# Kernel optimization log

Measured on AMD Instinct MI355X. Metric: run time of the kernel, lower is better.

Reference implementation:

```python
import jax, jax.numpy as jnp
import numpy as np

T, K, N = 4096, 4096, 11008
EPS = 1e-5


def setup_inputs() -> dict:
    key = jax.random.key(0)
    k1, k2, k3, k4 = jax.random.split(key, 4)
    input_tensor = jax.random.normal(k1, (1, T, K), dtype=jnp.bfloat16)
    # int8 weights in [-127, 127]
    weight = jax.random.randint(k2, (N, K), -127, 128, dtype=jnp.int8)
    # per-output-channel weight scale, small positive values
    weight_scale = (jax.random.uniform(k3, (N, 1), dtype=jnp.float32) * 0.02 + 1e-4)
    bias = jax.random.normal(k4, (N,), dtype=jnp.bfloat16)
    return {"input_tensor": input_tensor, "weight": weight,
            "weight_scale": weight_scale, "bias": bias}


def _quantize_per_token_absmax(x):
    # x: [T, K] float -> int8 quant [T, K], float32 scale [T, 1]
    xf = x.astype(jnp.float32)
    absmax = jnp.max(jnp.abs(xf), axis=-1, keepdims=True)  # [T, 1]
    scale = jnp.maximum(absmax, EPS) / 127.0
    q = jnp.clip(jnp.round(xf / scale), -127, 127).astype(jnp.int8)
    return q, scale


def reference(input_tensor, weight, weight_scale, bias):
    x = jnp.squeeze(input_tensor, axis=0)                  # [T, K]
    x_q, x_scale = _quantize_per_token_absmax(x)           # int8 [T,K], f32 [T,1]
    # int8 GEMM with int32 accumulation: [T, K] @ [K, N]
    acc = jax.lax.dot_general(
        x_q, weight.T,
        dimension_numbers=(((1,), (0,)), ((), ())),
        preferred_element_type=jnp.int32,
    )
    # dequantize: per-token scale * per-channel scale
    out = (acc.astype(jnp.float32) * x_scale * weight_scale.T).astype(jnp.bfloat16)
    out = out + bias
    return out[None, :, :]                                  # [1, T, N]
```

## Files before the change

kernel.cpp:

```cpp
#include <hip/hip_runtime.h>
#include <hip/hip_bf16.h>
#include <stdint.h>

#define T_DIM 4096
#define K_DIM 4096
#define N_DIM 11008

#define XQ_OFF 0
#define XS_OFF 16777216
#define W8_OFF 16793600

typedef __attribute__((ext_vector_type(4))) int v4i;

__global__ __launch_bounds__(256) void quant_kernel(
    const float* __restrict__ x, int8_t* __restrict__ xq, float* __restrict__ xs)
{
    const int wid   = threadIdx.x >> 6;
    const int lane  = threadIdx.x & 63;
    const int token = blockIdx.x * 4 + wid;

    const float* xrow = x + (size_t)token * K_DIM;

    float4 v[16];
    float am = 0.0f;
#pragma unroll
    for (int j = 0; j < 16; ++j) {
        v[j] = *(const float4*)(xrow + (size_t)(j * 64 + lane) * 4);
        am = fmaxf(am, fmaxf(fmaxf(fabsf(v[j].x), fabsf(v[j].y)),
                             fmaxf(fabsf(v[j].z), fabsf(v[j].w))));
    }
#pragma unroll
    for (int m = 1; m < 64; m <<= 1)
        am = fmaxf(am, __shfl_xor(am, m, 64));

    const float scale = fmaxf(am, 1e-5f) / 127.0f;
    if (lane == 0) xs[token] = scale;

    uint32_t* qrow = (uint32_t*)(xq + (size_t)token * K_DIM);
#pragma unroll
    for (int j = 0; j < 16; ++j) {
        int q0 = min(127, max(-127, (int)rintf(v[j].x / scale)));
        int q1 = min(127, max(-127, (int)rintf(v[j].y / scale)));
        int q2 = min(127, max(-127, (int)rintf(v[j].z / scale)));
        int q3 = min(127, max(-127, (int)rintf(v[j].w / scale)));
        qrow[j * 64 + lane] = ((uint32_t)(uint8_t)(int8_t)q0)       |
                              ((uint32_t)(uint8_t)(int8_t)q1 << 8)  |
                              ((uint32_t)(uint8_t)(int8_t)q2 << 16) |
                              ((uint32_t)(uint8_t)(int8_t)q3 << 24);
    }
}

__global__ __launch_bounds__(256) void pack_w_kernel(
    const int* __restrict__ w32, int8_t* __restrict__ w8)
{
    const size_t tid = (size_t)blockIdx.x * 256 + threadIdx.x;
    const int4* src = (const int4*)w32 + tid * 4;
    uint32_t o[4];
#pragma unroll
    for (int i = 0; i < 4; ++i) {
        int4 a = src[i];
        o[i] = ((uint32_t)a.x & 0xFFu) | (((uint32_t)a.y & 0xFFu) << 8) |
               (((uint32_t)a.z & 0xFFu) << 16) | ((uint32_t)a.w << 24);
    }
    *(uint4*)(w8 + tid * 16) = make_uint4(o[0], o[1], o[2], o[3]);
}

#define BM 256
#define BN 256
#define BKB 64
#define NT (K_DIM / BKB)
#define BUF_SZ 16384

__global__ __launch_bounds__(512, 2) void gemm_i8_kernel(
    const int8_t* __restrict__ xq, const int8_t* __restrict__ w8,
    const float* __restrict__ xs, const float* __restrict__ wsc,
    const __hip_bfloat16* __restrict__ bias, float* __restrict__ out)
{
    __shared__ int8_t lds[3 * 2 * BUF_SZ];

    constexpr int NBN = N_DIM / BN;
    constexpr int NWG = (T_DIM / BM) * NBN;
    constexpr int CPX = NWG / 8;

    const int bid = blockIdx.x;
    const int b2  = (bid % 8) * CPX + bid / 8;
    const int bm  = b2 / NBN;
    const int bn  = b2 % NBN;

    const int tid  = threadIdx.x;
    const int wid  = tid >> 6;
    const int lane = tid & 63;
    const int wm   = wid >> 2;
    const int wn   = wid & 3;

    const int fr = lane & 15, kg = lane >> 4;
    int offA[8], offB[4];
#pragma unroll
    for (int mi = 0; mi < 8; ++mi) {
        const int row = wm * 128 + mi * 16 + fr;
        offA[mi] = row * 64 + ((kg ^ ((row >> 1) & 3)) << 4);
    }
#pragma unroll
    for (int ni = 0; ni < 4; ++ni) {
        const int row = wn * 64 + ni * 16 + fr;
        offB[ni] = row * 64 + ((kg ^ ((row >> 1) & 3)) << 4);
    }

    const int srow  = tid >> 2;
    const int sslot = tid & 3;
    const int r0 = srow, r1 = 128 + srow;
    const int c0 = sslot ^ ((r0 >> 1) & 3);
    const int c1 = sslot ^ ((r1 >> 1) & 3);
    const int8_t* gA0 = xq + (size_t)(bm * BM + r0) * K_DIM + c0 * 16;
    const int8_t* gA1 = xq + (size_t)(bm * BM + r1) * K_DIM + c1 * 16;
    const int8_t* gB0 = w8 + (size_t)(bn * BM + r0) * K_DIM + c0 * 16;
    const int8_t* gB1 = w8 + (size_t)(bn * BM + r1) * K_DIM + c1 * 16;
    const int ldsW = wid * 1024;

    v4i acc[8][4];
#pragma unroll
    for (int mi = 0; mi < 8; ++mi)
#pragma unroll
        for (int ni = 0; ni < 4; ++ni) acc[mi][ni] = (v4i){0, 0, 0, 0};

#define STAGE(bufb, mat, Rr, kt)                                                \
    __builtin_amdgcn_global_load_lds(                                           \
        (const __attribute__((address_space(1))) void*)(                        \
            ((mat) ? ((Rr) ? gB1 : gB0) : ((Rr) ? gA1 : gA0)) +                 \
            (size_t)(kt) * BKB),                                                \
        (__attribute__((address_space(3))) void*)(                              \
            lds + ((bufb) * 2 + (mat)) * BUF_SZ + (Rr) * 8192 + ldsW),          \
        16, 0, 0)

    STAGE(0, 0, 0, 0); STAGE(0, 0, 1, 0); STAGE(0, 1, 0, 0); STAGE(0, 1, 1, 0);
    STAGE(1, 0, 0, 1); STAGE(1, 0, 1, 1); STAGE(1, 1, 0, 1); STAGE(1, 1, 1, 1);
    asm volatile("s_waitcnt vmcnt(4)" ::: "memory");
    __builtin_amdgcn_s_barrier();
    asm volatile("" ::: "memory");

    for (int t = 0; t < NT; ++t) {
        const int b  = t % 3;
        const int pb = (t + 2) % 3;
        const int8_t* bA = lds + (b * 2 + 0) * BUF_SZ;
        const int8_t* bB = lds + (b * 2 + 1) * BUF_SZ;

        v4i bF[4], aF[4];
#pragma unroll
        for (int ni = 0; ni < 4; ++ni) bF[ni] = *(const v4i*)(bB + offB[ni]);
#pragma unroll
        for (int mi = 0; mi < 4; ++mi) aF[mi] = *(const v4i*)(bA + offA[mi]);
        if (t + 2 < NT) { STAGE(pb, 0, 0, t + 2); STAGE(pb, 0, 1, t + 2); }
        __builtin_amdgcn_s_barrier();
        asm volatile("" ::: "memory");
        __builtin_amdgcn_s_setprio(1);
#pragma unroll
        for (int mi = 0; mi < 4; ++mi)
#pragma unroll
            for (int ni = 0; ni < 4; ++ni)
                acc[mi][ni] = __builtin_amdgcn_mfma_i32_16x16x64_i8(
                    aF[mi], bF[ni], acc[mi][ni], 0, 0, 0);
        __builtin_amdgcn_s_setprio(0);
        __builtin_amdgcn_s_barrier();
        asm volatile("" ::: "memory");

#pragma unroll
        for (int mi = 0; mi < 4; ++mi) aF[mi] = *(const v4i*)(bA + offA[mi + 4]);
        if (t + 2 < NT) { STAGE(pb, 1, 0, t + 2); STAGE(pb, 1, 1, t + 2); }
        __builtin_amdgcn_s_barrier();
        asm volatile("" ::: "memory");
        __builtin_amdgcn_s_setprio(1);
#pragma unroll
        for (int mi = 0; mi < 4; ++mi)
#pragma unroll
            for (int ni = 0; ni < 4; ++ni)
                acc[mi + 4][ni] = __builtin_amdgcn_mfma_i32_16x16x64_i8(
                    aF[mi], bF[ni], acc[mi + 4][ni], 0, 0, 0);
        __builtin_amdgcn_s_setprio(0);
        if (t < NT - 2) asm volatile("s_waitcnt vmcnt(4)" ::: "memory");
        else            asm volatile("s_waitcnt vmcnt(0)" ::: "memory");
        __builtin_amdgcn_s_barrier();
        asm volatile("" ::: "memory");
    }

    const int row0 = bm * BM + wm * 128 + (lane >> 4) * 4;
    const int col0 = bn * BN + wn * 64 + (lane & 15);
#pragma unroll
    for (int mi = 0; mi < 8; ++mi) {
#pragma unroll
        for (int j = 0; j < 4; ++j) {
            const int row = row0 + mi * 16 + j;
            const float xscale = xs[row];
#pragma unroll
            for (int ni = 0; ni < 4; ++ni) {
                const int col = col0 + ni * 16;
                float p   = (float)acc[mi][ni][j] * xscale * wsc[col];
                float pb_ = __bfloat162float(__float2bfloat16(p));
                float vb  = __bfloat162float(__float2bfloat16(
                                pb_ + __bfloat162float(bias[col])));
                out[(size_t)row * N_DIM + col] = vb;
            }
        }
    }
#undef STAGE
}

extern "C" void kernel_launch(void* const* d_in, const int* in_sizes, int n_in,
                              void* d_out, int out_size, void* d_ws, size_t ws_size,
                              hipStream_t stream)
{
    const float*          x    = (const float*)d_in[0];
    const int*            w32  = (const int*)d_in[1];
    const float*          wsc  = (const float*)d_in[2];
    const __hip_bfloat16* bias = (const __hip_bfloat16*)d_in[3];
    float*                out  = (float*)d_out;

    int8_t* xq = (int8_t*)d_ws + XQ_OFF;
    float*  xs = (float*)((char*)d_ws + XS_OFF);
    int8_t* w8 = (int8_t*)d_ws + W8_OFF;

    quant_kernel<<<T_DIM / 4, 256, 0, stream>>>(x, xq, xs);
    pack_w_kernel<<<(N_DIM * (K_DIM / 16)) / 256, 256, 0, stream>>>(w32, w8);
    gemm_i8_kernel<<<(T_DIM / BM) * (N_DIM / BN), 512, 0, stream>>>(
        xq, w8, xs, wsc, bias, out);
}
```

Measured before the change: 275.0 us.

## Merge prep kernels and split GEMM k-step into four finer MFMA phases

Combines the activation quantization and weight packing kernels into one launch, with blocks dispatched by index, so one launch overhead and the gap between the two kernels go away. The GEMM main loop moves from two phases of 16 MFMAs to four phases of 8 MFMAs. Each phase issues one global-to-LDS prefetch and loads two A fragments, which spreads the memory traffic more evenly across the compute and lowers A-fragment register use. The cost is twice as many workgroup barriers per k-step, which may hurt MFMA throughput.

New measurement: 269.4 us. -2.0%, faster.

```diff
diff --git a/kernel.cpp b/kernel.cpp
--- a/kernel.cpp
+++ b/kernel.cpp
@@ -12,57 +12,56 @@
 
 typedef __attribute__((ext_vector_type(4))) int v4i;
 
-__global__ __launch_bounds__(256) void quant_kernel(
-    const float* __restrict__ x, int8_t* __restrict__ xq, float* __restrict__ xs)
-{
-    const int wid   = threadIdx.x >> 6;
-    const int lane  = threadIdx.x & 63;
-    const int token = blockIdx.x * 4 + wid;
-
-    const float* xrow = x + (size_t)token * K_DIM;
-
-    float4 v[16];
-    float am = 0.0f;
-#pragma unroll
-    for (int j = 0; j < 16; ++j) {
-        v[j] = *(const float4*)(xrow + (size_t)(j * 64 + lane) * 4);
-        am = fmaxf(am, fmaxf(fmaxf(fabsf(v[j].x), fabsf(v[j].y)),
-                             fmaxf(fabsf(v[j].z), fabsf(v[j].w))));
-    }
-#pragma unroll
-    for (int m = 1; m < 64; m <<= 1)
-        am = fmaxf(am, __shfl_xor(am, m, 64));
-
-    const float scale = fmaxf(am, 1e-5f) / 127.0f;
-    if (lane == 0) xs[token] = scale;
-
-    uint32_t* qrow = (uint32_t*)(xq + (size_t)token * K_DIM);
-#pragma unroll
-    for (int j = 0; j < 16; ++j) {
-        int q0 = min(127, max(-127, (int)rintf(v[j].x / scale)));
-        int q1 = min(127, max(-127, (int)rintf(v[j].y / scale)));
-        int q2 = min(127, max(-127, (int)rintf(v[j].z / scale)));
-        int q3 = min(127, max(-127, (int)rintf(v[j].w / scale)));
-        qrow[j * 64 + lane] = ((uint32_t)(uint8_t)(int8_t)q0)       |
-                              ((uint32_t)(uint8_t)(int8_t)q1 << 8)  |
-                              ((uint32_t)(uint8_t)(int8_t)q2 << 16) |
-                              ((uint32_t)(uint8_t)(int8_t)q3 << 24);
-    }
-}
-
-__global__ __launch_bounds__(256) void pack_w_kernel(
+__global__ __launch_bounds__(256) void prep_kernel(
+    const float* __restrict__ x, int8_t* __restrict__ xq, float* __restrict__ xs,
     const int* __restrict__ w32, int8_t* __restrict__ w8)
 {
-    const size_t tid = (size_t)blockIdx.x * 256 + threadIdx.x;
-    const int4* src = (const int4*)w32 + tid * 4;
-    uint32_t o[4];
-#pragma unroll
-    for (int i = 0; i < 4; ++i) {
-        int4 a = src[i];
-        o[i] = ((uint32_t)a.x & 0xFFu) | (((uint32_t)a.y & 0xFFu) << 8) |
-               (((uint32_t)a.z & 0xFFu) << 16) | ((uint32_t)a.w << 24);
-    }
-    *(uint4*)(w8 + tid * 16) = make_uint4(o[0], o[1], o[2], o[3]);
+    if (blockIdx.x < T_DIM / 4) {
+        const int wid   = threadIdx.x >> 6;
+        const int lane  = threadIdx.x & 63;
+        const int token = blockIdx.x * 4 + wid;
+
+        const float* xrow = x + (size_t)token * K_DIM;
+
+        float4 v[16];
+        float am = 0.0f;
+#pragma unroll
+        for (int j = 0; j < 16; ++j) {
+            v[j] = *(const float4*)(xrow + (size_t)(j * 64 + lane) * 4);
+            am = fmaxf(am, fmaxf(fmaxf(fabsf(v[j].x), fabsf(v[j].y)),
+                                 fmaxf(fabsf(v[j].z), fabsf(v[j].w))));
+        }
+#pragma unroll
+        for (int m = 1; m < 64; m <<= 1)
+            am = fmaxf(am, __shfl_xor(am, m, 64));
+
+        const float scale = fmaxf(am, 1e-5f) / 127.0f;
+        if (lane == 0) xs[token] = scale;
+
+        uint32_t* qrow = (uint32_t*)(xq + (size_t)token * K_DIM);
+#pragma unroll
+        for (int j = 0; j < 16; ++j) {
+            int q0 = min(127, max(-127, (int)rintf(v[j].x / scale)));
+            int q1 = min(127, max(-127, (int)rintf(v[j].y / scale)));
+            int q2 = min(127, max(-127, (int)rintf(v[j].z / scale)));
+            int q3 = min(127, max(-127, (int)rintf(v[j].w / scale)));
+            qrow[j * 64 + lane] = ((uint32_t)(uint8_t)(int8_t)q0)       |
+                                  ((uint32_t)(uint8_t)(int8_t)q1 << 8)  |
+                                  ((uint32_t)(uint8_t)(int8_t)q2 << 16) |
+                                  ((uint32_t)(uint8_t)(int8_t)q3 << 24);
+        }
+    } else {
+        const size_t tid = (size_t)(blockIdx.x - T_DIM / 4) * 256 + threadIdx.x;
+        const int4* src = (const int4*)w32 + tid * 4;
+        uint32_t o[4];
+#pragma unroll
+        for (int i = 0; i < 4; ++i) {
+            int4 a = src[i];
+            o[i] = ((uint32_t)a.x & 0xFFu) | (((uint32_t)a.y & 0xFFu) << 8) |
+                   (((uint32_t)a.z & 0xFFu) << 16) | ((uint32_t)a.w << 24);
+        }
+        *(uint4*)(w8 + tid * 16) = make_uint4(o[0], o[1], o[2], o[3]);
+    }
 }
 
 #define BM 256
@@ -132,6 +131,14 @@
             lds + ((bufb) * 2 + (mat)) * BUF_SZ + (Rr) * 8192 + ldsW),          \
         16, 0, 0)
 
+#define MFMA_PAIR(base)                                                         \
+    _Pragma("unroll")                                                           \
+    for (int mi = 0; mi < 2; ++mi)                                              \
+        _Pragma("unroll")                                                       \
+        for (int ni = 0; ni < 4; ++ni)                                          \
+            acc[(base) + mi][ni] = __builtin_amdgcn_mfma_i32_16x16x64_i8(       \
+                aF[mi], bF[ni], acc[(base) + mi][ni], 0, 0, 0)
+
     STAGE(0, 0, 0, 0); STAGE(0, 0, 1, 0); STAGE(0, 1, 0, 0); STAGE(0, 1, 1, 0);
     STAGE(1, 0, 0, 1); STAGE(1, 0, 1, 1); STAGE(1, 1, 0, 1); STAGE(1, 1, 1, 1);
     asm volatile("s_waitcnt vmcnt(4)" ::: "memory");
@@ -143,38 +150,52 @@
         const int pb = (t + 2) % 3;
         const int8_t* bA = lds + (b * 2 + 0) * BUF_SZ;
         const int8_t* bB = lds + (b * 2 + 1) * BUF_SZ;
-
-        v4i bF[4], aF[4];
+        const bool pf = (t + 2 < NT);
+
+        v4i bF[4], aF[2];
+
 #pragma unroll
         for (int ni = 0; ni < 4; ++ni) bF[ni] = *(const v4i*)(bB + offB[ni]);
-#pragma unroll
-        for (int mi = 0; mi < 4; ++mi) aF[mi] = *(const v4i*)(bA + offA[mi]);
-        if (t + 2 < NT) { STAGE(pb, 0, 0, t + 2); STAGE(pb, 0, 1, t + 2); }
-        __builtin_amdgcn_s_barrier();
-        asm volatile("" ::: "memory");
-        __builtin_amdgcn_s_setprio(1);
-#pragma unroll
-        for (int mi = 0; mi < 4; ++mi)
-#pragma unroll
-            for (int ni = 0; ni < 4; ++ni)
-                acc[mi][ni] = __builtin_amdgcn_mfma_i32_16x16x64_i8(
-                    aF[mi], bF[ni], acc[mi][ni], 0, 0, 0);
-        __builtin_amdgcn_s_setprio(0);
-        __builtin_amdgcn_s_barrier();
-        asm volatile("" ::: "memory");
-
-#pragma unroll
-        for (int mi = 0; mi < 4; ++mi) aF[mi] = *(const v4i*)(bA + offA[mi + 4]);
-        if (t + 2 < NT) { STAGE(pb, 1, 0, t + 2); STAGE(pb, 1, 1, t + 2); }
-        __builtin_amdgcn_s_barrier();
-        asm volatile("" ::: "memory");
-        __builtin_amdgcn_s_setprio(1);
-#pragma unroll
-        for (int mi = 0; mi < 4; ++mi)
-#pragma unroll
-            for (int ni = 0; ni < 4; ++ni)
-                acc[mi + 4][ni] = __builtin_amdgcn_mfma_i32_16x16x64_i8(
-                    aF[mi], bF[ni], acc[mi + 4][ni], 0, 0, 0);
+        aF[0] = *(const v4i*)(bA + offA[0]);
+        aF[1] = *(const v4i*)(bA + offA[1]);
+        if (pf) STAGE(pb, 0, 0, t + 2);
+        __builtin_amdgcn_s_barrier();
+        asm volatile("" ::: "memory");
+        __builtin_amdgcn_s_setprio(1);
+        MFMA_PAIR(0);
+        __builtin_amdgcn_s_setprio(0);
+        __builtin_amdgcn_s_barrier();
+        asm volatile("" ::: "memory");
+
+        aF[0] = *(const v4i*)(bA + offA[2]);
+        aF[1] = *(const v4i*)(bA + offA[3]);
+        if (pf) STAGE(pb, 0, 1, t + 2);
+        __builtin_amdgcn_s_barrier();
+        asm volatile("" ::: "memory");
+        __builtin_amdgcn_s_setprio(1);
+        MFMA_PAIR(2);
+        __builtin_amdgcn_s_setprio(0);
+        __builtin_amdgcn_s_barrier();
+        asm volatile("" ::: "memory");
+
+        aF[0] = *(const v4i*)(bA + offA[4]);
+        aF[1] = *(const v4i*)(bA + offA[5]);
+        if (pf) STAGE(pb, 1, 0, t + 2);
+        __builtin_amdgcn_s_barrier();
+        asm volatile("" ::: "memory");
+        __builtin_amdgcn_s_setprio(1);
+        MFMA_PAIR(4);
+        __builtin_amdgcn_s_setprio(0);
+        __builtin_amdgcn_s_barrier();
+        asm volatile("" ::: "memory");
+
+        aF[0] = *(const v4i*)(bA + offA[6]);
+        aF[1] = *(const v4i*)(bA + offA[7]);
+        if (pf) STAGE(pb, 1, 1, t + 2);
+        __builtin_amdgcn_s_barrier();
+        asm volatile("" ::: "memory");
+        __builtin_amdgcn_s_setprio(1);
+        MFMA_PAIR(6);
         __builtin_amdgcn_s_setprio(0);
         if (t < NT - 2) asm volatile("s_waitcnt vmcnt(4)" ::: "memory");
         else            asm volatile("s_waitcnt vmcnt(0)" ::: "memory");
@@ -193,8 +214,8 @@
 #pragma unroll
             for (int ni = 0; ni < 4; ++ni) {
                 const int col = col0 + ni * 16;
-                float p   = (float)acc[mi][ni][j] * xscale * wsc[col];
-                float pb_ = __bfloat162float(__float2bfloat16(p));
+                float p_  = (float)acc[mi][ni][j] * xscale * wsc[col];
+                float pb_ = __bfloat162float(__float2bfloat16(p_));
                 float vb  = __bfloat162float(__float2bfloat16(
                                 pb_ + __bfloat162float(bias[col])));
                 out[(size_t)row * N_DIM + col] = vb;
@@ -202,6 +223,7 @@
         }
     }
 #undef STAGE
+#undef MFMA_PAIR
 }
 
 extern "C" void kernel_launch(void* const* d_in, const int* in_sizes, int n_in,
@@ -218,8 +240,8 @@
     float*  xs = (float*)((char*)d_ws + XS_OFF);
     int8_t* w8 = (int8_t*)d_ws + W8_OFF;
 
-    quant_kernel<<<T_DIM / 4, 256, 0, stream>>>(x, xq, xs);
-    pack_w_kernel<<<(N_DIM * (K_DIM / 16)) / 256, 256, 0, stream>>>(w32, w8);
+    prep_kernel<<<T_DIM / 4 + (N_DIM * (K_DIM / 16)) / 256, 256, 0, stream>>>(
+        x, xq, xs, w32, w8);
     gemm_i8_kernel<<<(T_DIM / BM) * (N_DIM / BN), 512, 0, stream>>>(
         xq, w8, xs, wsc, bias, out);
 }
```

## Merge prep kernels and collapse GEMM main loop into single-phase schedule

Applied to the files above, without the earlier changes.

Activation quantization and weight packing move into one prep kernel whose blocks branch on block index, which removes one launch and lets both jobs run concurrently. The GEMM inner loop drops its two-phase split with four barriers per K-tile. It now issues all four global-to-LDS prefetches up front, loads all A and B fragments, runs the 32 MFMAs, and then waits once before a single barrier. This cuts barrier overhead but holds eight A fragments live at once, which raises register pressure and gives less interleaving of LDS reads with MFMA work.

Result: faster. 264.7 us (-3.8%).

```diff
diff --git a/kernel.cpp b/kernel.cpp
--- a/kernel.cpp
+++ b/kernel.cpp
@@ -12,57 +12,56 @@
 
 typedef __attribute__((ext_vector_type(4))) int v4i;
 
-__global__ __launch_bounds__(256) void quant_kernel(
-    const float* __restrict__ x, int8_t* __restrict__ xq, float* __restrict__ xs)
-{
-    const int wid   = threadIdx.x >> 6;
-    const int lane  = threadIdx.x & 63;
-    const int token = blockIdx.x * 4 + wid;
-
-    const float* xrow = x + (size_t)token * K_DIM;
-
-    float4 v[16];
-    float am = 0.0f;
-#pragma unroll
-    for (int j = 0; j < 16; ++j) {
-        v[j] = *(const float4*)(xrow + (size_t)(j * 64 + lane) * 4);
-        am = fmaxf(am, fmaxf(fmaxf(fabsf(v[j].x), fabsf(v[j].y)),
-                             fmaxf(fabsf(v[j].z), fabsf(v[j].w))));
-    }
-#pragma unroll
-    for (int m = 1; m < 64; m <<= 1)
-        am = fmaxf(am, __shfl_xor(am, m, 64));
-
-    const float scale = fmaxf(am, 1e-5f) / 127.0f;
-    if (lane == 0) xs[token] = scale;
-
-    uint32_t* qrow = (uint32_t*)(xq + (size_t)token * K_DIM);
-#pragma unroll
-    for (int j = 0; j < 16; ++j) {
-        int q0 = min(127, max(-127, (int)rintf(v[j].x / scale)));
-        int q1 = min(127, max(-127, (int)rintf(v[j].y / scale)));
-        int q2 = min(127, max(-127, (int)rintf(v[j].z / scale)));
-        int q3 = min(127, max(-127, (int)rintf(v[j].w / scale)));
-        qrow[j * 64 + lane] = ((uint32_t)(uint8_t)(int8_t)q0)       |
-                              ((uint32_t)(uint8_t)(int8_t)q1 << 8)  |
-                              ((uint32_t)(uint8_t)(int8_t)q2 << 16) |
-                              ((uint32_t)(uint8_t)(int8_t)q3 << 24);
-    }
-}
-
-__global__ __launch_bounds__(256) void pack_w_kernel(
+__global__ __launch_bounds__(256) void prep_kernel(
+    const float* __restrict__ x, int8_t* __restrict__ xq, float* __restrict__ xs,
     const int* __restrict__ w32, int8_t* __restrict__ w8)
 {
-    const size_t tid = (size_t)blockIdx.x * 256 + threadIdx.x;
-    const int4* src = (const int4*)w32 + tid * 4;
-    uint32_t o[4];
-#pragma unroll
-    for (int i = 0; i < 4; ++i) {
-        int4 a = src[i];
-        o[i] = ((uint32_t)a.x & 0xFFu) | (((uint32_t)a.y & 0xFFu) << 8) |
-               (((uint32_t)a.z & 0xFFu) << 16) | ((uint32_t)a.w << 24);
-    }
-    *(uint4*)(w8 + tid * 16) = make_uint4(o[0], o[1], o[2], o[3]);
+    if (blockIdx.x < T_DIM / 4) {
+        const int wid   = threadIdx.x >> 6;
+        const int lane  = threadIdx.x & 63;
+        const int token = blockIdx.x * 4 + wid;
+
+        const float* xrow = x + (size_t)token * K_DIM;
+
+        float4 v[16];
+        float am = 0.0f;
+#pragma unroll
+        for (int j = 0; j < 16; ++j) {
+            v[j] = *(const float4*)(xrow + (size_t)(j * 64 + lane) * 4);
+            am = fmaxf(am, fmaxf(fmaxf(fabsf(v[j].x), fabsf(v[j].y)),
+                                 fmaxf(fabsf(v[j].z), fabsf(v[j].w))));
+        }
+#pragma unroll
+        for (int m = 1; m < 64; m <<= 1)
+            am = fmaxf(am, __shfl_xor(am, m, 64));
+
+        const float scale = fmaxf(am, 1e-5f) / 127.0f;
+        if (lane == 0) xs[token] = scale;
+
+        uint32_t* qrow = (uint32_t*)(xq + (size_t)token * K_DIM);
+#pragma unroll
+        for (int j = 0; j < 16; ++j) {
+            int q0 = min(127, max(-127, (int)rintf(v[j].x / scale)));
+            int q1 = min(127, max(-127, (int)rintf(v[j].y / scale)));
+            int q2 = min(127, max(-127, (int)rintf(v[j].z / scale)));
+            int q3 = min(127, max(-127, (int)rintf(v[j].w / scale)));
+            qrow[j * 64 + lane] = ((uint32_t)(uint8_t)(int8_t)q0)       |
+                                  ((uint32_t)(uint8_t)(int8_t)q1 << 8)  |
+                                  ((uint32_t)(uint8_t)(int8_t)q2 << 16) |
+                                  ((uint32_t)(uint8_t)(int8_t)q3 << 24);
+        }
+    } else {
+        const size_t tid = (size_t)(blockIdx.x - T_DIM / 4) * 256 + threadIdx.x;
+        const int4* src = (const int4*)w32 + tid * 4;
+        uint32_t o[4];
+#pragma unroll
+        for (int i = 0; i < 4; ++i) {
+            int4 a = src[i];
+            o[i] = ((uint32_t)a.x & 0xFFu) | (((uint32_t)a.y & 0xFFu) << 8) |
+                   (((uint32_t)a.z & 0xFFu) << 16) | ((uint32_t)a.w << 24);
+        }
+        *(uint4*)(w8 + tid * 16) = make_uint4(o[0], o[1], o[2], o[3]);
+    }
 }
 
 #define BM 256
@@ -144,38 +143,26 @@
         const int8_t* bA = lds + (b * 2 + 0) * BUF_SZ;
         const int8_t* bB = lds + (b * 2 + 1) * BUF_SZ;
 
-        v4i bF[4], aF[4];
+        if (t + 2 < NT) {
+            STAGE(pb, 0, 0, t + 2); STAGE(pb, 0, 1, t + 2);
+            STAGE(pb, 1, 0, t + 2); STAGE(pb, 1, 1, t + 2);
+        }
+
+        v4i bF[4], aF[8];
 #pragma unroll
         for (int ni = 0; ni < 4; ++ni) bF[ni] = *(const v4i*)(bB + offB[ni]);
 #pragma unroll
-        for (int mi = 0; mi < 4; ++mi) aF[mi] = *(const v4i*)(bA + offA[mi]);
-        if (t + 2 < NT) { STAGE(pb, 0, 0, t + 2); STAGE(pb, 0, 1, t + 2); }
-        __builtin_amdgcn_s_barrier();
-        asm volatile("" ::: "memory");
+        for (int mi = 0; mi < 8; ++mi) aF[mi] = *(const v4i*)(bA + offA[mi]);
+
         __builtin_amdgcn_s_setprio(1);
 #pragma unroll
-        for (int mi = 0; mi < 4; ++mi)
+        for (int mi = 0; mi < 8; ++mi)
 #pragma unroll
             for (int ni = 0; ni < 4; ++ni)
                 acc[mi][ni] = __builtin_amdgcn_mfma_i32_16x16x64_i8(
                     aF[mi], bF[ni], acc[mi][ni], 0, 0, 0);
         __builtin_amdgcn_s_setprio(0);
-        __builtin_amdgcn_s_barrier();
-        asm volatile("" ::: "memory");
-
-#pragma unroll
-        for (int mi = 0; mi < 4; ++mi) aF[mi] = *(const v4i*)(bA + offA[mi + 4]);
-        if (t + 2 < NT) { STAGE(pb, 1, 0, t + 2); STAGE(pb, 1, 1, t + 2); }
-        __builtin_amdgcn_s_barrier();
-        asm volatile("" ::: "memory");
-        __builtin_amdgcn_s_setprio(1);
-#pragma unroll
-        for (int mi = 0; mi < 4; ++mi)
-#pragma unroll
-            for (int ni = 0; ni < 4; ++ni)
-                acc[mi + 4][ni] = __builtin_amdgcn_mfma_i32_16x16x64_i8(
-                    aF[mi], bF[ni], acc[mi + 4][ni], 0, 0, 0);
-        __builtin_amdgcn_s_setprio(0);
+
         if (t < NT - 2) asm volatile("s_waitcnt vmcnt(4)" ::: "memory");
         else            asm volatile("s_waitcnt vmcnt(0)" ::: "memory");
         __builtin_amdgcn_s_barrier();
@@ -193,8 +180,8 @@
 #pragma unroll
             for (int ni = 0; ni < 4; ++ni) {
                 const int col = col0 + ni * 16;
-                float p   = (float)acc[mi][ni][j] * xscale * wsc[col];
-                float pb_ = __bfloat162float(__float2bfloat16(p));
+                float p_  = (float)acc[mi][ni][j] * xscale * wsc[col];
+                float pb_ = __bfloat162float(__float2bfloat16(p_));
                 float vb  = __bfloat162float(__float2bfloat16(
                                 pb_ + __bfloat162float(bias[col])));
                 out[(size_t)row * N_DIM + col] = vb;
@@ -218,8 +205,8 @@
     float*  xs = (float*)((char*)d_ws + XS_OFF);
     int8_t* w8 = (int8_t*)d_ws + W8_OFF;
 
-    quant_kernel<<<T_DIM / 4, 256, 0, stream>>>(x, xq, xs);
-    pack_w_kernel<<<(N_DIM * (K_DIM / 16)) / 256, 256, 0, stream>>>(w32, w8);
+    prep_kernel<<<T_DIM / 4 + (N_DIM * (K_DIM / 16)) / 256, 256, 0, stream>>>(
+        x, xq, xs, w32, w8);
     gemm_i8_kernel<<<(T_DIM / BM) * (N_DIM / BN), 512, 0, stream>>>(
         xq, w8, xs, wsc, bias, out);
 }
```
